# Optimization experiments

Hardware: AMD Instinct MI355X
Metric: run time of the kernel (lower is better)

## Reference

```python
import jax, jax.numpy as jnp
import numpy as np

B, T = 16, 64
A = 6              # num_actions
E = 12288          # embed_size
DET = 4096         # deter_size
HID = 1024         # hidden_size
S, D = 32, 32      # stoch_size, discrete
UM = 0.01          # uniform_mix
CLIP = 1.0         # action_clip
EPS = 1e-3         # LayerNorm eps


def _ln(x, g, b):
    m = jnp.mean(x, -1, keepdims=True)
    v = jnp.var(x, -1, keepdims=True)
    return (x - m) * jax.lax.rsqrt(v + EPS) * g + b


def setup_inputs() -> dict:
    key = jax.random.key(0)
    ks = jax.random.split(key, 24)
    w = lambda k, i, o: (jax.random.normal(k, (i, o), jnp.float32) / np.sqrt(i))
    gum = lambda k, shp: -jnp.log(-jnp.log(jax.random.uniform(k, shp, jnp.float32, 1e-6, 1.0 - 1e-6)))
    is_firsts = (jax.random.uniform(ks[2], (B, T)) < 0.05).astype(jnp.float32)
    is_firsts = is_firsts.at[:, 0].set(1.0)
    return {
        'embed': jax.random.normal(ks[0], (B, T, E), jnp.float32),
        'prev_actions': jax.random.normal(ks[1], (B, T, A), jnp.float32),
        'is_firsts': is_firsts,
        'gumbel_prior': gum(ks[3], (B, T, S, D)),
        'gumbel_post': gum(ks[4], (B, T, S, D)),
        'w_init': jnp.zeros((DET,), jnp.float32),
        'W_img1': w(ks[5], S * D + A, HID), 'g_img1': jnp.ones((HID,)), 'b_img1': jnp.zeros((HID,)),
        'W_gru': w(ks[6], HID + DET, 3 * DET), 'g_gru': jnp.ones((3 * DET,)), 'b_gru': jnp.zeros((3 * DET,)),
        'W_img2a': w(ks[7], DET, HID), 'g_img2': jnp.ones((HID,)), 'b_img2': jnp.zeros((HID,)),
        'W_img2b': w(ks[8], HID, S * D), 'bb_img2': jnp.zeros((S * D,)),
        'W_obs': w(ks[9], E + DET, HID), 'g_obs': jnp.ones((HID,)), 'b_obs': jnp.zeros((HID,)),
        'W_obsb': w(ks[10], HID, S * D), 'bb_obs': jnp.zeros((S * D,)),
    }


def reference(embed, prev_actions, is_firsts, gumbel_prior, gumbel_post,
              w_init, W_img1, g_img1, b_img1, W_gru, g_gru, b_gru,
              W_img2a, g_img2, b_img2, W_img2b, bb_img2,
              W_obs, g_obs, b_obs, W_obsb, bb_obs):
    sg = jax.lax.stop_gradient

    def clip_act(a):
        return a * sg(CLIP / jnp.maximum(jnp.abs(a), CLIP))

    def prior_logits(deter):  # mlp_img2
        h = jax.nn.silu(_ln(deter @ W_img2a, g_img2, b_img2))
        return (h @ W_img2b + bb_img2).reshape(deter.shape[:-1] + (S, D))

    def mix_probs(logits):  # OneHotDist uniform mix
        p = jax.nn.softmax(logits, -1)
        return (1.0 - UM) * p + UM / D

    def st_sample(logits, g):  # straight-through gumbel-max sample
        p = mix_probs(logits)
        oh = jax.nn.one_hot(jnp.argmax(jnp.log(p) + g, -1), D, dtype=logits.dtype)
        return oh + p - sg(p)

    def st_mode(logits):
        p = mix_probs(logits)
        oh = jax.nn.one_hot(jnp.argmax(p, -1), D, dtype=logits.dtype)
        return oh + p - sg(p)

    # learned initial state (initial(): deter=tanh(w), stoch=mode, logits=0)
    init_deter = jnp.broadcast_to(jnp.tanh(w_init)[None], (B, DET))
    init_stoch = st_mode(prior_logits(init_deter))

    # observe() with prev_state=None zeroes the first action and starts from initial state
    prev_actions = prev_actions.at[:, 0].set(0.0)

    def step(carry, xs):
        stoch, deter, logits_post = carry
        a, e, f, gp, gq = xs
        a = clip_act(a)                                  # clip in forward()
        f1 = f[:, None]
        f3 = f[:, None, None]
        a = a * (1.0 - f1)
        stoch = stoch * (1.0 - f3) + init_stoch * f3
        deter = deter * (1.0 - f1) + init_deter * f1
        logits_post = logits_post * (1.0 - f3)           # initial logits are zeros
        a = clip_act(a)                                  # clipped again in forward_img()
        # mlp_img1
        x = jax.nn.silu(_ln(jnp.concatenate([stoch.reshape(B, S * D), a], -1) @ W_img1, g_img1, b_img1))
        # DreamerV2 GRU cell: single LN-linear -> reset/cand/update
        parts = _ln(jnp.concatenate([x, deter], -1) @ W_gru, g_gru, b_gru)
        reset, cand, update = jnp.split(parts, 3, -1)
        reset = jax.nn.sigmoid(reset)
        cand = jnp.tanh(reset * cand)
        update = jax.nn.sigmoid(update - 1.0)
        deter_new = update * cand + (1.0 - update) * deter
        # prior head
        lp = prior_logits(deter_new)
        stoch_prior = st_sample(lp, gp)
        # posterior head (mlp_obs1)
        h2 = jax.nn.silu(_ln(jnp.concatenate([e, deter_new], -1) @ W_obs, g_obs, b_obs))
        lq = (h2 @ W_obsb + bb_obs).reshape(B, S, D)
        stoch_post = st_sample(lq, gq)
        return (stoch_post, deter_new, lq), (stoch_post, deter_new, lq, stoch_prior, lp)

    carry0 = (init_stoch, init_deter, jnp.zeros((B, S, D), embed.dtype))
    xs = (jnp.swapaxes(prev_actions, 0, 1), jnp.swapaxes(embed, 0, 1), jnp.swapaxes(is_firsts, 0, 1),
          jnp.swapaxes(gumbel_prior, 0, 1), jnp.swapaxes(gumbel_post, 0, 1))
    _, outs = jax.lax.scan(step, carry0, xs)
    post_stoch, post_deter, post_logits, prior_stoch, prior_lg = [jnp.swapaxes(o, 0, 1) for o in outs]
    # pack posts and priors (prior deter == post deter) into one array [B,T,8192]
    return jnp.concatenate([post_stoch.reshape(B, T, S * D), post_deter,
                            post_logits.reshape(B, T, S * D),
                            prior_stoch.reshape(B, T, S * D),
                            prior_lg.reshape(B, T, S * D)], -1)
```

## Files before the change

### kernel.cpp

```cpp
#include <hip/hip_runtime.h>
#include <cmath>


#define B 16
#define T_STEPS 64
#define A_DIM 6
#define E_DIM 12288
#define DET 4096
#define HID 1024
#define SD 1024
#define OUT_C 8192
#define OUT_RSTRIDE (T_STEPS * OUT_C)

typedef float f2v __attribute__((ext_vector_type(2)));

__device__ __forceinline__ float block_sum(float v, float* red, int nw) {
#pragma unroll
  for (int m = 32; m >= 1; m >>= 1) v += __shfl_xor(v, m, 64);
  int wid = threadIdx.x >> 6;
  if ((threadIdx.x & 63) == 0) red[wid] = v;
  __syncthreads();
  if (wid == 0) {
    float s = ((int)threadIdx.x < nw) ? red[threadIdx.x] : 0.0f;
#pragma unroll
    for (int m = 8; m >= 1; m >>= 1) s += __shfl_xor(s, m, 16);
    if (threadIdx.x == 0) red[0] = s;
  }
  __syncthreads();
  float out = red[0];
  __syncthreads();
  return out;
}

__global__ __launch_bounds__(1024) void k_tanh(const float* __restrict__ w, float* __restrict__ o) {
  int i = blockIdx.x * 1024 + threadIdx.x;
  if (i < DET) o[i] = tanhf(w[i]);
}

__global__ __launch_bounds__(256) void k_prep(
    const float* __restrict__ isf, const float* __restrict__ pa, int t,
    const float* __restrict__ stoch_prev,
    const float* __restrict__ deter_prev, long deter_prev_stride,
    const float* __restrict__ init_stoch, const float* __restrict__ init_deter_row,
    float* __restrict__ stoch_in, float* __restrict__ deter_in, float* __restrict__ a_eff) {
  int r = blockIdx.x;
  float f = isf[r * T_STEPS + t];
  float omf = 1.0f - f;
  for (int c = threadIdx.x; c < SD; c += 256)
    stoch_in[r * SD + c] = stoch_prev[r * SD + c] * omf + init_stoch[r * SD + c] * f;
  for (int c = threadIdx.x; c < DET; c += 256)
    deter_in[r * DET + c] = deter_prev[(long)r * deter_prev_stride + c] * omf + init_deter_row[c] * f;
  if ((int)threadIdx.x < A_DIM) {
    float a = pa[(r * T_STEPS + t) * A_DIM + threadIdx.x];
    a = a * (1.0f / fmaxf(fabsf(a), 1.0f));
    a_eff[r * 8 + threadIdx.x] = a * omf;
  }
}

struct GemmArgs {
  const float* A0; long sA0; int cA0;
  const float* A1; long sA1;
  const float* W; int N; int Ktot; int KS; int nsplit;
  float* P;
};

template <bool NT>
__global__ __launch_bounds__(256) void k_gemm(GemmArgs ga, GemmArgs gb) {
  const GemmArgs g = blockIdx.z ? gb : ga;
  if ((int)blockIdx.y >= g.nsplit) return;
  const int tid = threadIdx.x;
  const int c0 = blockIdx.x * 512 + tid * 2;
  const int k0 = (int)blockIdx.y * g.KS;
  __shared__ float in_s[16][64];
  float acc[16][2];
#pragma unroll
  for (int r = 0; r < 16; r++) { acc[r][0] = 0.f; acc[r][1] = 0.f; }
  for (int kb = 0; kb < g.KS; kb += 64) {
    const int kbase = k0 + kb;
#pragma unroll
    for (int j = 0; j < 4; j++) {
      int ii = tid + j * 256;
      int r = ii >> 6, kk = ii & 63;
      int k = kbase + kk;
      float v = 0.f;
      if (k < g.cA0) v = g.A0[(long)r * g.sA0 + k];
      else if (k < g.Ktot) v = g.A1[(long)r * g.sA1 + (k - g.cA0)];
      in_s[r][kk] = v;
    }
    __syncthreads();
    if (kbase + 64 <= g.Ktot) {
      const float* wp = g.W + (size_t)kbase * g.N + c0;
#pragma unroll 4
      for (int kk = 0; kk < 64; kk++) {
        f2v w = NT ? __builtin_nontemporal_load((const f2v*)wp) : *(const f2v*)wp;
        wp += g.N;
#pragma unroll
        for (int r = 0; r < 16; r++) {
          float iv = in_s[r][kk];
          acc[r][0] += iv * w[0]; acc[r][1] += iv * w[1];
        }
      }
    } else {
#pragma unroll 4
      for (int kk = 0; kk < 64; kk++) {
        int krow = kbase + kk; if (krow >= g.Ktot) krow = g.Ktot - 1;
        const f2v w = *(const f2v*)(g.W + (size_t)krow * g.N + c0);
#pragma unroll
        for (int r = 0; r < 16; r++) {
          float iv = in_s[r][kk];
          acc[r][0] += iv * w[0]; acc[r][1] += iv * w[1];
        }
      }
    }
    __syncthreads();
  }
#pragma unroll
  for (int r = 0; r < 16; r++)
    *(f2v*)(g.P + ((size_t)blockIdx.y * 16 + r) * g.N + c0) = f2v{acc[r][0], acc[r][1]};
}

__global__ __launch_bounds__(256) void k_pre(const float* __restrict__ A,
                                             const float* __restrict__ Bw,
                                             float* __restrict__ ob) {
  __shared__ float As[32][68];
  __shared__ float Bs[32][68];
  const int tid = threadIdx.x;
  const int tx = tid & 15, ty = tid >> 4;
  const int row0 = blockIdx.y * 64, col0 = blockIdx.x * 64;
  const int ar = tid >> 2, ak = (tid & 3) * 8;
  const int bk = tid >> 4, bc = (tid & 15) * 4;
  float acc[4][4] = {};
  const float* ap = A + (size_t)(row0 + ar) * E_DIM + ak;
  const float* bp = Bw + (size_t)bk * HID + col0 + bc;
  for (int k0 = 0; k0 < E_DIM; k0 += 32) {
    float4 a0 = *(const float4*)(ap + k0);
    float4 a1 = *(const float4*)(ap + k0 + 4);
    float4 b0 = *(const float4*)(bp + (size_t)k0 * HID);
    float4 b1 = *(const float4*)(bp + (size_t)(k0 + 16) * HID);
    __syncthreads();
    As[ak + 0][ar] = a0.x; As[ak + 1][ar] = a0.y; As[ak + 2][ar] = a0.z; As[ak + 3][ar] = a0.w;
    As[ak + 4][ar] = a1.x; As[ak + 5][ar] = a1.y; As[ak + 6][ar] = a1.z; As[ak + 7][ar] = a1.w;
    *(float4*)&Bs[bk][bc] = b0;
    *(float4*)&Bs[bk + 16][bc] = b1;
    __syncthreads();
#pragma unroll
    for (int kk = 0; kk < 32; kk++) {
      float4 av = *(const float4*)&As[kk][ty * 4];
      float4 bv = *(const float4*)&Bs[kk][tx * 4];
      acc[0][0] += av.x * bv.x; acc[0][1] += av.x * bv.y; acc[0][2] += av.x * bv.z; acc[0][3] += av.x * bv.w;
      acc[1][0] += av.y * bv.x; acc[1][1] += av.y * bv.y; acc[1][2] += av.y * bv.z; acc[1][3] += av.y * bv.w;
      acc[2][0] += av.z * bv.x; acc[2][1] += av.z * bv.y; acc[2][2] += av.z * bv.z; acc[2][3] += av.z * bv.w;
      acc[3][0] += av.w * bv.x; acc[3][1] += av.w * bv.y; acc[3][2] += av.w * bv.z; acc[3][3] += av.w * bv.w;
    }
  }
#pragma unroll
  for (int i = 0; i < 4; i++)
#pragma unroll
    for (int j = 0; j < 4; j++)
      ob[(size_t)(row0 + ty * 4 + i) * OUT_C + col0 + tx * 4 + j] = acc[i][j];
}

__global__ __launch_bounds__(256) void k_red(const float* __restrict__ P, int nP,
                                             float* __restrict__ S,
                                             float* __restrict__ red_s, float* __restrict__ red_q) {
  int chunk = blockIdx.x, r = blockIdx.y;
  int c = chunk * 1024 + threadIdx.x * 4;
  float4 s = {0, 0, 0, 0};
  for (int ks = 0; ks < nP; ks++) {
    float4 v = *(const float4*)(P + ((size_t)ks * 16 + r) * (3 * DET) + c);
    s.x += v.x; s.y += v.y; s.z += v.z; s.w += v.w;
  }
  *(float4*)(S + (size_t)r * (3 * DET) + c) = s;
  float sx = (s.x + s.y) + (s.z + s.w);
  float sq = (s.x * s.x + s.y * s.y) + (s.z * s.z + s.w * s.w);
  __shared__ float rbuf[8];
#pragma unroll
  for (int m = 32; m >= 1; m >>= 1) { sx += __shfl_xor(sx, m, 64); sq += __shfl_xor(sq, m, 64); }
  int wid = threadIdx.x >> 6;
  if ((threadIdx.x & 63) == 0) { rbuf[wid] = sx; rbuf[4 + wid] = sq; }
  __syncthreads();
  if (threadIdx.x == 0) {
    red_s[r * 12 + chunk] = (rbuf[0] + rbuf[1]) + (rbuf[2] + rbuf[3]);
    red_q[r * 12 + chunk] = (rbuf[4] + rbuf[5]) + (rbuf[6] + rbuf[7]);
  }
}

__global__ __launch_bounds__(1024) void k_gru_gate(
    const float* __restrict__ S, const float* __restrict__ red_s, const float* __restrict__ red_q,
    const float* __restrict__ g, const float* __restrict__ b,
    float* __restrict__ deter_in, float* __restrict__ deter_new,
    float* __restrict__ out_deter, const float* __restrict__ isf, int t,
    const float* __restrict__ init_deter) {
  int r = blockIdx.x;
  __shared__ float mv[2];
  if (threadIdx.x == 0) {
    float s = 0.f, q = 0.f;
    for (int k2 = 0; k2 < 12; k2++) { s += red_s[r * 12 + k2]; q += red_q[r * 12 + k2]; }
    float m = s * (1.0f / (float)(3 * DET));
    float var = q * (1.0f / (float)(3 * DET)) - m * m;
    mv[0] = m; mv[1] = 1.0f / sqrtf(var + 1e-3f);
  }
  __syncthreads();
  float m = mv[0], rs = mv[1];
  float ft = (t + 1 < T_STEPS) ? isf[r * T_STEPS + t + 1] : 0.0f;
  for (int j = threadIdx.x; j < DET; j += 1024) {
    float lr = (S[(size_t)r * (3 * DET) + j] - m) * rs * g[j] + b[j];
    float lc = (S[(size_t)r * (3 * DET) + j + DET] - m) * rs * g[j + DET] + b[j + DET];
    float lu = (S[(size_t)r * (3 * DET) + j + 2 * DET] - m) * rs * g[j + 2 * DET] + b[j + 2 * DET];
    float rr = 1.0f / (1.0f + expf(-lr));
    float cd = tanhf(rr * lc);
    float uu = 1.0f / (1.0f + expf(-(lu - 1.0f)));
    float dn = uu * cd + (1.0f - uu) * deter_in[r * DET + j];
    deter_new[r * DET + j] = dn;
    out_deter[(size_t)r * OUT_RSTRIDE + j] = dn;
    deter_in[r * DET + j] = dn * (1.0f - ft) + init_deter[j] * ft;
  }
}

__global__ __launch_bounds__(1024) void k_fin2(
    const float* __restrict__ Pa_, int nPa, const float* __restrict__ addA, long adsA,
    const float* __restrict__ gva, const float* __restrict__ bva, float* __restrict__ oa,
    const float* __restrict__ Pb_, int nPb, const float* __restrict__ addB, long adsB,
    const float* __restrict__ gvb, const float* __restrict__ bvb, float* __restrict__ ob) {
  int which = blockIdx.x >> 4, r = blockIdx.x & 15, c = threadIdx.x;
  const float* P = which ? Pb_ : Pa_;
  int nP = which ? nPb : nPa;
  const float* add = which ? addB : addA;
  long ads = which ? adsB : adsA;
  const float* gv = which ? gvb : gva;
  const float* bv = which ? bvb : bva;
  float* o = which ? ob : oa;
  __shared__ float red[18];
  float v = add ? add[(size_t)r * ads + c] : 0.0f;
  for (int ks = 0; ks < nP; ks++) v += P[((size_t)ks * 16 + r) * HID + c];
  float m = block_sum(v, red, 16) * (1.0f / (float)HID);
  float d = v - m;
  float var = block_sum(d * d, red, 16) * (1.0f / (float)HID);
  float rs = 1.0f / sqrtf(var + 1e-3f);
  float y = d * rs * gv[c] + bv[c];
  float s = 1.0f / (1.0f + expf(-y));
  o[r * HID + c] = y * s;
}

__global__ __launch_bounds__(1024) void k_samp(
    const float* __restrict__ P0, const float* __restrict__ bb0,
    const float* __restrict__ gum0, long gs0,
    float* __restrict__ st0, long ss0, float* __restrict__ lg0, long ls0,
    const float* __restrict__ P1, const float* __restrict__ bb1,
    const float* __restrict__ gum1, long gs1,
    float* __restrict__ st1, long ss1, float* __restrict__ lg1, long ls1,
    int nP,
    const float* __restrict__ isf, const float* __restrict__ pa, int t,
    float* __restrict__ stoch_in, float* __restrict__ a_eff,
    const float* __restrict__ init_stoch) {
  int which = blockIdx.x >> 4, r = blockIdx.x & 15, c = threadIdx.x;
  const float* P = which ? P1 : P0;
  const float* bbv = which ? bb1 : bb0;
  const float* gum = which ? gum1 : gum0;
  long gs = which ? gs1 : gs0;
  float* st = which ? st1 : st0;
  long ss = which ? ss1 : ss0;
  float* lg = which ? lg1 : lg0;
  long ls = which ? ls1 : ls0;
  float acc = bbv[c];
  for (int ks = 0; ks < nP; ks++) acc += P[((size_t)ks * 16 + r) * SD + c];
  int d = c & 31;
  float mx = acc;
#pragma unroll
  for (int m = 16; m >= 1; m >>= 1) mx = fmaxf(mx, __shfl_xor(mx, m, 32));
  float e = expf(acc - mx);
  float se = e;
#pragma unroll
  for (int m = 16; m >= 1; m >>= 1) se += __shfl_xor(se, m, 32);
  float p = 0.99f * (e / se) + 3.125e-4f;
  float y = gum ? (logf(p) + gum[(long)r * gs + c]) : p;
  float by = y; int bi = d;
#pragma unroll
  for (int m = 16; m >= 1; m >>= 1) {
    float oy = __shfl_xor(by, m, 32);
    int oi = __shfl_xor(bi, m, 32);
    if (oy > by || (oy == by && oi < bi)) { by = oy; bi = oi; }
  }
  float oh = (d == bi) ? 1.0f : 0.0f;
  float outv = (oh + p) - p;
  st[(long)r * ss + c] = outv;
  if (lg) lg[(long)r * ls + c] = acc;
  if (which && stoch_in) {
    float fn = (t + 1 < T_STEPS) ? isf[r * T_STEPS + t + 1] : 0.0f;
    stoch_in[r * SD + c] = outv * (1.0f - fn) + init_stoch[r * SD + c] * fn;
    if (c < A_DIM) {
      float a = (t + 1 < T_STEPS) ? pa[(r * T_STEPS + t + 1) * A_DIM + c] : 0.0f;
      a = a * (1.0f / fmaxf(fabsf(a), 1.0f));
      a_eff[r * 8 + c] = a * (1.0f - fn);
    }
  }
}

static inline GemmArgs mkargs(const float* A0, long sA0, int cA0,
                              const float* A1, long sA1,
                              const float* W, int N, int Ktot, int KS, int nsplit, float* P) {
  GemmArgs g; g.A0 = A0; g.sA0 = sA0; g.cA0 = cA0; g.A1 = A1; g.sA1 = sA1;
  g.W = W; g.N = N; g.Ktot = Ktot; g.KS = KS; g.nsplit = nsplit; g.P = P;
  return g;
}

extern "C" void kernel_launch(void* const* d_in, const int* in_sizes, int n_in,
                              void* d_out, int out_size, void* d_ws, size_t ws_size,
                              hipStream_t stream) {
  const float* embed  = (const float*)d_in[0];
  const float* pa     = (const float*)d_in[1];
  const float* isf    = (const float*)d_in[2];
  const float* gprior = (const float*)d_in[3];
  const float* gpost  = (const float*)d_in[4];
  const float* w_init = (const float*)d_in[5];
  const float* W1  = (const float*)d_in[6];
  const float* g1  = (const float*)d_in[7];
  const float* b1  = (const float*)d_in[8];
  const float* Wg  = (const float*)d_in[9];
  const float* gg  = (const float*)d_in[10];
  const float* bg  = (const float*)d_in[11];
  const float* W2a = (const float*)d_in[12];
  const float* g2  = (const float*)d_in[13];
  const float* b2  = (const float*)d_in[14];
  const float* W2b = (const float*)d_in[15];
  const float* bb2 = (const float*)d_in[16];
  const float* Wo  = (const float*)d_in[17];
  const float* go  = (const float*)d_in[18];
  const float* bo  = (const float*)d_in[19];
  const float* Wob = (const float*)d_in[20];
  const float* bbo = (const float*)d_in[21];
  float* out = (float*)d_out;
  float* ws  = (float*)d_ws;

  float* Pg    = ws;
  float* Sg    = Pg + 3932160;
  float* red_s = Sg + 196608;
  float* red_q = red_s + 192;
  float* Pa    = red_s + 512;
  float* Pb    = Pa + 524288;
  float* Ps0   = Pb + 524288;
  float* Ps1   = Ps0 + 262144;
  float* Pimg1 = Pa;
  float* st_   = Ps1 + 262144;
  float* init_stoch = st_;
  float* init_deter = st_ + 16384;
  float* stoch_in   = st_ + 20480;
  float* deter_in   = st_ + 36864;
  float* deter_new  = st_ + 102400;
  float* a_eff      = st_ + 167936;
  float* x          = st_ + 168064;
  float* h          = st_ + 184448;
  float* h2         = st_ + 200832;

  GemmArgs Z = mkargs(nullptr, 0, 0, nullptr, 0, nullptr, 1, 0, 64, 0, nullptr);

  k_pre<<<dim3(16, 16), 256, 0, stream>>>(embed, Wo, out + 5120);

  k_tanh<<<4, 1024, 0, stream>>>(w_init, init_deter);
  {
    GemmArgs g = mkargs(init_deter, 0, DET, nullptr, 0, W2a, HID, DET, 128, 32, Pa);
    k_gemm<true><<<dim3(2, 32, 1), 256, 0, stream>>>(g, Z);
  }
  k_fin2<<<16, 1024, 0, stream>>>(Pa, 32, nullptr, 0, g2, b2, h,
                                  Pa, 32, nullptr, 0, g2, b2, h);
  {
    GemmArgs g = mkargs(h, HID, HID, nullptr, 0, W2b, SD, HID, 64, 16, Ps0);
    k_gemm<true><<<dim3(2, 16, 1), 256, 0, stream>>>(g, Z);
  }
  k_samp<<<16, 1024, 0, stream>>>(Ps0, bb2, nullptr, 0, init_stoch, SD, nullptr, 0,
                                  Ps0, bb2, nullptr, 0, init_stoch, SD, nullptr, 0,
                                  16, isf, pa, -1, nullptr, nullptr, init_stoch);

  k_prep<<<16, 256, 0, stream>>>(isf, pa, 0, init_stoch, init_deter, 0,
                                 init_stoch, init_deter, stoch_in, deter_in, a_eff);

  for (int t = 0; t < T_STEPS; t++) {
    {
      GemmArgs g = mkargs(stoch_in, SD, SD, a_eff, 8, W1, HID, SD + A_DIM, 64, 17, Pimg1);
      k_gemm<true><<<dim3(2, 17, 1), 256, 0, stream>>>(g, Z);
    }
    k_fin2<<<16, 1024, 0, stream>>>(Pimg1, 17, nullptr, 0, g1, b1, x,
                                    Pimg1, 17, nullptr, 0, g1, b1, x);
    {
      GemmArgs g = mkargs(x, HID, HID, deter_in, DET, Wg, 3 * DET, HID + DET, 256, 20, Pg);
      k_gemm<false><<<dim3(24, 20, 1), 256, 0, stream>>>(g, Z);
    }
    k_red<<<dim3(12, 16), 256, 0, stream>>>(Pg, 20, Sg, red_s, red_q);
    k_gru_gate<<<16, 1024, 0, stream>>>(Sg, red_s, red_q, gg, bg, deter_in, deter_new,
                                        out + (size_t)t * OUT_C + 1024, isf, t, init_deter);
    {
      GemmArgs gp = mkargs(deter_new, DET, DET, nullptr, 0, W2a, HID, DET, 128, 32, Pa);
      GemmArgs go_ = mkargs(deter_new, DET, DET, nullptr, 0, Wo + (size_t)E_DIM * HID,
                            HID, DET, 128, 32, Pb);
      k_gemm<true><<<dim3(2, 32, 2), 256, 0, stream>>>(gp, go_);
    }
    k_fin2<<<32, 1024, 0, stream>>>(Pa, 32, nullptr, 0, g2, b2, h,
                                    Pb, 32, out + (size_t)t * OUT_C + 5120, OUT_RSTRIDE,
                                    go, bo, h2);
    {
      GemmArgs gs0 = mkargs(h, HID, HID, nullptr, 0, W2b, SD, HID, 64, 16, Ps0);
      GemmArgs gs1 = mkargs(h2, HID, HID, nullptr, 0, Wob, SD, HID, 64, 16, Ps1);
      k_gemm<true><<<dim3(2, 16, 2), 256, 0, stream>>>(gs0, gs1);
    }
    k_samp<<<32, 1024, 0, stream>>>(
        Ps0, bb2, gprior + (size_t)t * SD, (long)T_STEPS * SD,
        out + (size_t)t * OUT_C + 6144, OUT_RSTRIDE,
        out + (size_t)t * OUT_C + 7168, OUT_RSTRIDE,
        Ps1, bbo, gpost + (size_t)t * SD, (long)T_STEPS * SD,
        out + (size_t)t * OUT_C + 0, OUT_RSTRIDE,
        out + (size_t)t * OUT_C + 5120, OUT_RSTRIDE,
        16, isf, pa, t, stoch_in, a_eff, init_stoch);
  }
}
```

Baseline: 10.94 ms.

## Hoist prior head out of recurrent loop into batched post-loop GEMMs

The prior head (W_img2a, LayerNorm, W_img2b and prior sampling) does not feed back into the recurrence, so it is taken out of the per-step loop. After the loop it runs as batched tiled GEMMs over all 1024 (B*T) rows, reading deter from the output buffer. This removes half the per-step weight streaming for the prior path and fuses per-row work into large efficient GEMMs. The GEMM kernel also moves its barrier to the top of the k-loop, raises its unroll factor, and drops the dual-argument dispatch.

```diff
diff --git a/kernel.cpp b/kernel.cpp
--- a/kernel.cpp
+++ b/kernel.cpp
@@ -13,6 +13,7 @@
 #define OUT_RSTRIDE (T_STEPS * OUT_C)
 
 typedef float f2v __attribute__((ext_vector_type(2)));
+typedef float f4v __attribute__((ext_vector_type(4)));
 
 __device__ __forceinline__ float block_sum(float v, float* red, int nw) {
 #pragma unroll
@@ -65,9 +66,7 @@
 };
 
 template <bool NT>
-__global__ __launch_bounds__(256) void k_gemm(GemmArgs ga, GemmArgs gb) {
-  const GemmArgs g = blockIdx.z ? gb : ga;
-  if ((int)blockIdx.y >= g.nsplit) return;
+__global__ __launch_bounds__(256) void k_gemm(GemmArgs g) {
   const int tid = threadIdx.x;
   const int c0 = blockIdx.x * 512 + tid * 2;
   const int k0 = (int)blockIdx.y * g.KS;
@@ -77,6 +76,7 @@
   for (int r = 0; r < 16; r++) { acc[r][0] = 0.f; acc[r][1] = 0.f; }
   for (int kb = 0; kb < g.KS; kb += 64) {
     const int kbase = k0 + kb;
+    __syncthreads();
 #pragma unroll
     for (int j = 0; j < 4; j++) {
       int ii = tid + j * 256;
@@ -90,38 +90,79 @@
     __syncthreads();
     if (kbase + 64 <= g.Ktot) {
       const float* wp = g.W + (size_t)kbase * g.N + c0;
-#pragma unroll 4
+#pragma unroll 8
       for (int kk = 0; kk < 64; kk++) {
         f2v w = NT ? __builtin_nontemporal_load((const f2v*)wp) : *(const f2v*)wp;
         wp += g.N;
 #pragma unroll
         for (int r = 0; r < 16; r++) {
-          float iv = in_s[r][kk];
-          acc[r][0] += iv * w[0]; acc[r][1] += iv * w[1];
+          acc[r][0] += in_s[r][kk] * w[0]; acc[r][1] += in_s[r][kk] * w[1];
         }
       }
     } else {
-#pragma unroll 4
       for (int kk = 0; kk < 64; kk++) {
         int krow = kbase + kk; if (krow >= g.Ktot) krow = g.Ktot - 1;
         const f2v w = *(const f2v*)(g.W + (size_t)krow * g.N + c0);
 #pragma unroll
         for (int r = 0; r < 16; r++) {
-          float iv = in_s[r][kk];
-          acc[r][0] += iv * w[0]; acc[r][1] += iv * w[1];
+          acc[r][0] += in_s[r][kk] * w[0]; acc[r][1] += in_s[r][kk] * w[1];
         }
       }
     }
-    __syncthreads();
   }
 #pragma unroll
   for (int r = 0; r < 16; r++)
     *(f2v*)(g.P + ((size_t)blockIdx.y * 16 + r) * g.N + c0) = f2v{acc[r][0], acc[r][1]};
 }
 
-__global__ __launch_bounds__(256) void k_pre(const float* __restrict__ A,
-                                             const float* __restrict__ Bw,
-                                             float* __restrict__ ob) {
+__global__ __launch_bounds__(1024) void k_fin(
+    const float* __restrict__ P, int nP,
+    const float* __restrict__ add, long ads,
+    const float* __restrict__ gv, const float* __restrict__ bv,
+    float* __restrict__ o) {
+  int r = blockIdx.x, c = threadIdx.x;
+  __shared__ float red[18];
+  float v = add ? add[(size_t)r * ads + c] : 0.0f;
+  for (int ks = 0; ks < nP; ks++) v += P[((size_t)ks * 16 + r) * HID + c];
+  float m = block_sum(v, red, 16) * (1.0f / (float)HID);
+  float d = v - m;
+  float var = block_sum(d * d, red, 16) * (1.0f / (float)HID);
+  float rs = 1.0f / sqrtf(var + 1e-3f);
+  float y = d * rs * gv[c] + bv[c];
+  float s = 1.0f / (1.0f + expf(-y));
+  o[r * HID + c] = y * s;
+}
+
+__global__ __launch_bounds__(1024) void k_samp_init(
+    const float* __restrict__ P, int nP, const float* __restrict__ bb,
+    float* __restrict__ st) {
+  int r = blockIdx.x, c = threadIdx.x;
+  float acc = bb[c];
+  for (int ks = 0; ks < nP; ks++) acc += P[((size_t)ks * 16 + r) * SD + c];
+  int d = c & 31;
+  float mx = acc;
+#pragma unroll
+  for (int m = 16; m >= 1; m >>= 1) mx = fmaxf(mx, __shfl_xor(mx, m, 32));
+  float e = expf(acc - mx);
+  float se = e;
+#pragma unroll
+  for (int m = 16; m >= 1; m >>= 1) se += __shfl_xor(se, m, 32);
+  float p = 0.99f * (e / se) + 3.125e-4f;
+  float by = p; int bi = d;
+#pragma unroll
+  for (int m = 16; m >= 1; m >>= 1) {
+    float oy = __shfl_xor(by, m, 32);
+    int oi = __shfl_xor(bi, m, 32);
+    if (oy > by || (oy == by && oi < bi)) { by = oy; bi = oi; }
+  }
+  float oh = (d == bi) ? 1.0f : 0.0f;
+  st[r * SD + c] = (oh + p) - p;
+}
+
+__global__ __launch_bounds__(256) void k_mm(const float* __restrict__ A, long lda,
+                                            const float* __restrict__ Bw, int K,
+                                            float* __restrict__ out, long ldo,
+                                            const float* __restrict__ bias) {
   __shared__ float As[32][68];
   __shared__ float Bs[32][68];
   const int tid = threadIdx.x;
@@ -130,9 +171,9 @@
   const int ar = tid >> 2, ak = (tid & 3) * 8;
   const int bk = tid >> 4, bc = (tid & 15) * 4;
   float acc[4][4] = {};
-  const float* ap = A + (size_t)(row0 + ar) * E_DIM + ak;
+  const float* ap = A + (size_t)(row0 + ar) * lda + ak;
   const float* bp = Bw + (size_t)bk * HID + col0 + bc;
-  for (int k0 = 0; k0 < E_DIM; k0 += 32) {
+  for (int k0 = 0; k0 < K; k0 += 32) {
     float4 a0 = *(const float4*)(ap + k0);
     float4 a1 = *(const float4*)(ap + k0 + 4);
     float4 b0 = *(const float4*)(bp + (size_t)k0 * HID);
@@ -154,10 +195,60 @@
     }
   }
 #pragma unroll
-  for (int i = 0; i < 4; i++)
-#pragma unroll
-    for (int j = 0; j < 4; j++)
-      ob[(size_t)(row0 + ty * 4 + i) * OUT_C + col0 + tx * 4 + j] = acc[i][j];
+  for (int i = 0; i < 4; i++) {
+    float4 o;
+    int col = col0 + tx * 4;
+    o.x = acc[i][0] + (bias ? bias[col + 0] : 0.f);
+    o.y = acc[i][1] + (bias ? bias[col + 1] : 0.f);
+    o.z = acc[i][2] + (bias ? bias[col + 2] : 0.f);
+    o.w = acc[i][3] + (bias ? bias[col + 3] : 0.f);
+    *(float4*)(out + (size_t)(row0 + ty * 4 + i) * ldo + col) = o;
+  }
+}
+
+__global__ __launch_bounds__(256) void k_ln_rows(float* __restrict__ h,
+                                                 const float* __restrict__ gv,
+                                                 const float* __restrict__ bv) {
+  int row = blockIdx.x, c0 = threadIdx.x * 4;
+  __shared__ float red[18];
+  float4 v = *(const float4*)(h + (size_t)row * HID + c0);
+  float lsum = (v.x + v.y) + (v.z + v.w);
+  float m = block_sum(lsum, red, 4) * (1.0f / (float)HID);
+  float dx = v.x - m, dy = v.y - m, dz = v.z - m, dw = v.w - m;
+  float lv = (dx * dx + dy * dy) + (dz * dz + dw * dw);
+  float var = block_sum(lv, red, 4) * (1.0f / (float)HID);
+  float rs = 1.0f / sqrtf(var + 1e-3f);
+  float4 o;
+  float y0 = dx * rs * gv[c0] + bv[c0];         o.x = y0 / (1.0f + expf(-y0));
+  float y1 = dy * rs * gv[c0 + 1] + bv[c0 + 1]; o.y = y1 / (1.0f + expf(-y1));
+  float y2 = dz * rs * gv[c0 + 2] + bv[c0 + 2]; o.z = y2 / (1.0f + expf(-y2));
+  float y3 = dw * rs * gv[c0 + 3] + bv[c0 + 3]; o.w = y3 / (1.0f + expf(-y3));
+  *(float4*)(h + (size_t)row * HID + c0) = o;
+}
+
+__global__ __launch_bounds__(1024) void k_samp_prior(float* __restrict__ out,
+                                                     const float* __restrict__ gum) {
+  int m = blockIdx.x, c = threadIdx.x;
+  float lp = out[(size_t)m * OUT_C + 7168 + c];
+  int d = c & 31;
+  float mx = lp;
+#pragma unroll
+  for (int mm = 16; mm >= 1; mm >>= 1) mx = fmaxf(mx, __shfl_xor(mx, mm, 32));
+  float e = expf(lp - mx);
+  float se = e;
+#pragma unroll
+  for (int mm = 16; mm >= 1; mm >>= 1) se += __shfl_xor(se, mm, 32);
+  float p = 0.99f * (e / se) + 3.125e-4f;
+  float y = logf(p) + gum[(size_t)m * SD + c];
+  float by = y; int bi = d;
+#pragma unroll
+  for (int mm = 16; mm >= 1; mm >>= 1) {
+    float oy = __shfl_xor(by, mm, 32);
+    int oi = __shfl_xor(bi, mm, 32);
+    if (oy > by || (oy == by && oi < bi)) { by = oy; bi = oi; }
+  }
+  float oh = (d == bi) ? 1.0f : 0.0f;
+  out[(size_t)m * OUT_C + 6144 + c] = (oh + p) - p;
 }
 
 __global__ __launch_bounds__(256) void k_red(const float* __restrict__ P, int nP,
@@ -217,52 +308,15 @@
   }
 }
 
-__global__ __launch_bounds__(1024) void k_fin2(
-    const float* __restrict__ Pa_, int nPa, const float* __restrict__ addA, long adsA,
-    const float* __restrict__ gva, const float* __restrict__ bva, float* __restrict__ oa,
-    const float* __restrict__ Pb_, int nPb, const float* __restrict__ addB, long adsB,
-    const float* __restrict__ gvb, const float* __restrict__ bvb, float* __restrict__ ob) {
-  int which = blockIdx.x >> 4, r = blockIdx.x & 15, c = threadIdx.x;
-  const float* P = which ? Pb_ : Pa_;
-  int nP = which ? nPb : nPa;
-  const float* add = which ? addB : addA;
-  long ads = which ? adsB : adsA;
-  const float* gv = which ? gvb : gva;
-  const float* bv = which ? bvb : bva;
-  float* o = which ? ob : oa;
-  __shared__ float red[18];
-  float v = add ? add[(size_t)r * ads + c] : 0.0f;
-  for (int ks = 0; ks < nP; ks++) v += P[((size_t)ks * 16 + r) * HID + c];
-  float m = block_sum(v, red, 16) * (1.0f / (float)HID);
-  float d = v - m;
-  float var = block_sum(d * d, red, 16) * (1.0f / (float)HID);
-  float rs = 1.0f / sqrtf(var + 1e-3f);
-  float y = d * rs * gv[c] + bv[c];
-  float s = 1.0f / (1.0f + expf(-y));
-  o[r * HID + c] = y * s;
-}
-
 __global__ __launch_bounds__(1024) void k_samp(
-    const float* __restrict__ P0, const float* __restrict__ bb0,
-    const float* __restrict__ gum0, long gs0,
-    float* __restrict__ st0, long ss0, float* __restrict__ lg0, long ls0,
-    const float* __restrict__ P1, const float* __restrict__ bb1,
-    const float* __restrict__ gum1, long gs1,
-    float* __restrict__ st1, long ss1, float* __restrict__ lg1, long ls1,
-    int nP,
+    const float* __restrict__ P, int nP, const float* __restrict__ bb,
+    const float* __restrict__ gum, long gs,
+    float* __restrict__ st, long ss, float* __restrict__ lg, long ls,
     const float* __restrict__ isf, const float* __restrict__ pa, int t,
     float* __restrict__ stoch_in, float* __restrict__ a_eff,
     const float* __restrict__ init_stoch) {
-  int which = blockIdx.x >> 4, r = blockIdx.x & 15, c = threadIdx.x;
-  const float* P = which ? P1 : P0;
-  const float* bbv = which ? bb1 : bb0;
-  const float* gum = which ? gum1 : gum0;
-  long gs = which ? gs1 : gs0;
-  float* st = which ? st1 : st0;
-  long ss = which ? ss1 : ss0;
-  float* lg = which ? lg1 : lg0;
-  long ls = which ? ls1 : ls0;
-  float acc = bbv[c];
+  int r = blockIdx.x, c = threadIdx.x;
+  float acc = bb[c];
   for (int ks = 0; ks < nP; ks++) acc += P[((size_t)ks * 16 + r) * SD + c];
   int d = c & 31;
   float mx = acc;
@@ -273,7 +327,7 @@
 #pragma unroll
   for (int m = 16; m >= 1; m >>= 1) se += __shfl_xor(se, m, 32);
   float p = 0.99f * (e / se) + 3.125e-4f;
-  float y = gum ? (logf(p) + gum[(long)r * gs + c]) : p;
+  float y = logf(p) + gum[(long)r * gs + c];
   float by = y; int bi = d;
 #pragma unroll
   for (int m = 16; m >= 1; m >>= 1) {
@@ -284,15 +338,13 @@
   float oh = (d == bi) ? 1.0f : 0.0f;
   float outv = (oh + p) - p;
   st[(long)r * ss + c] = outv;
-  if (lg) lg[(long)r * ls + c] = acc;
-  if (which && stoch_in) {
-    float fn = (t + 1 < T_STEPS) ? isf[r * T_STEPS + t + 1] : 0.0f;
-    stoch_in[r * SD + c] = outv * (1.0f - fn) + init_stoch[r * SD + c] * fn;
-    if (c < A_DIM) {
-      float a = (t + 1 < T_STEPS) ? pa[(r * T_STEPS + t + 1) * A_DIM + c] : 0.0f;
-      a = a * (1.0f / fmaxf(fabsf(a), 1.0f));
-      a_eff[r * 8 + c] = a * (1.0f - fn);
-    }
+  lg[(long)r * ls + c] = acc;
+  float fn = (t + 1 < T_STEPS) ? isf[r * T_STEPS + t + 1] : 0.0f;
+  stoch_in[r * SD + c] = outv * (1.0f - fn) + init_stoch[r * SD + c] * fn;
+  if (c < A_DIM) {
+    float a = (t + 1 < T_STEPS) ? pa[(r * T_STEPS + t + 1) * A_DIM + c] : 0.0f;
+    a = a * (1.0f / fmaxf(fabsf(a), 1.0f));
+    a_eff[r * 8 + c] = a * (1.0f - fn);
   }
 }
 
@@ -333,14 +385,13 @@
   float* ws  = (float*)d_ws;
 
   float* Pg    = ws;
+  float* h_all = Pg;
   float* Sg    = Pg + 3932160;
   float* red_s = Sg + 196608;
   float* red_q = red_s + 192;
-  float* Pa    = red_s + 512;
-  float* Pb    = Pa + 524288;
-  float* Ps0   = Pb + 524288;
-  float* Ps1   = Ps0 + 262144;
-  float* Pimg1 = Pa;
+  float* Pimg1 = red_s + 512;
+  float* Pb    = Pimg1 + 278528;
+  float* Ps1   = Pb + 524288;
   float* st_   = Ps1 + 262144;
   float* init_stoch = st_;
   float* init_deter = st_ + 16384;
@@ -349,66 +400,45 @@
   float* deter_new  = st_ + 102400;
   float* a_eff      = st_ + 167936;
   float* x          = st_ + 168064;
-  float* h          = st_ + 184448;
-  float* h2         = st_ + 200832;
-
-  GemmArgs Z = mkargs(nullptr, 0, 0, nullptr, 0, nullptr, 1, 0, 64, 0, nullptr);
-
-  k_pre<<<dim3(16, 16), 256, 0, stream>>>(embed, Wo, out + 5120);
+  float* h2         = st_ + 184448;
+
+  k_mm<<<dim3(16, 16), 256, 0, stream>>>(embed, E_DIM, Wo, E_DIM, out + 5120, OUT_C, nullptr);
 
   k_tanh<<<4, 1024, 0, stream>>>(w_init, init_deter);
-  {
-    GemmArgs g = mkargs(init_deter, 0, DET, nullptr, 0, W2a, HID, DET, 128, 32, Pa);
-    k_gemm<true><<<dim3(2, 32, 1), 256, 0, stream>>>(g, Z);
-  }
-  k_fin2<<<16, 1024, 0, stream>>>(Pa, 32, nullptr, 0, g2, b2, h,
-                                  Pa, 32, nullptr, 0, g2, b2, h);
-  {
-    GemmArgs g = mkargs(h, HID, HID, nullptr, 0, W2b, SD, HID, 64, 16, Ps0);
-    k_gemm<true><<<dim3(2, 16, 1), 256, 0, stream>>>(g, Z);
-  }
-  k_samp<<<16, 1024, 0, stream>>>(Ps0, bb2, nullptr, 0, init_stoch, SD, nullptr, 0,
-                                  Ps0, bb2, nullptr, 0, init_stoch, SD, nullptr, 0,
-                                  16, isf, pa, -1, nullptr, nullptr, init_stoch);
+  k_gemm<true><<<dim3(2, 32), 256, 0, stream>>>(
+      mkargs(init_deter, 0, DET, nullptr, 0, W2a, HID, DET, 128, 32, Pb));
+  k_fin<<<16, 1024, 0, stream>>>(Pb, 32, nullptr, 0, g2, b2, x);
+  k_gemm<true><<<dim3(2, 16), 256, 0, stream>>>(
+      mkargs(x, HID, HID, nullptr, 0, W2b, SD, HID, 64, 16, Ps1));
+  k_samp_init<<<16, 1024, 0, stream>>>(Ps1, 16, bb2, init_stoch);
 
   k_prep<<<16, 256, 0, stream>>>(isf, pa, 0, init_stoch, init_deter, 0,
                                  init_stoch, init_deter, stoch_in, deter_in, a_eff);
 
   for (int t = 0; t < T_STEPS; t++) {
-    {
-      GemmArgs g = mkargs(stoch_in, SD, SD, a_eff, 8, W1, HID, SD + A_DIM, 64, 17, Pimg1);
-      k_gemm<true><<<dim3(2, 17, 1), 256, 0, stream>>>(g, Z);
-    }
-    k_fin2<<<16, 1024, 0, stream>>>(Pimg1, 17, nullptr, 0, g1, b1, x,
-                                    Pimg1, 17, nullptr, 0, g1, b1, x);
-    {
-      GemmArgs g = mkargs(x, HID, HID, deter_in, DET, Wg, 3 * DET, HID + DET, 256, 20, Pg);
-      k_gemm<false><<<dim3(24, 20, 1), 256, 0, stream>>>(g, Z);
-    }
+    k_gemm<true><<<dim3(2, 17), 256, 0, stream>>>(
+        mkargs(stoch_in, SD, SD, a_eff, 8, W1, HID, SD + A_DIM, 64, 17, Pimg1));
+    k_fin<<<16, 1024, 0, stream>>>(Pimg1, 17, nullptr, 0, g1, b1, x);
+    k_gemm<false><<<dim3(24, 20), 256, 0, stream>>>(
+        mkargs(x, HID, HID, deter_in, DET, Wg, 3 * DET, HID + DET, 256, 20, Pg));
     k_red<<<dim3(12, 16), 256, 0, stream>>>(Pg, 20, Sg, red_s, red_q);
     k_gru_gate<<<16, 1024, 0, stream>>>(Sg, red_s, red_q, gg, bg, deter_in, deter_new,
                                         out + (size_t)t * OUT_C + 1024, isf, t, init_deter);
-    {
-      GemmArgs gp = mkargs(deter_new, DET, DET, nullptr, 0, W2a, HID, DET, 128, 32, Pa);
-      GemmArgs go_ = mkargs(deter_new, DET, DET, nullptr, 0, Wo + (size_t)E_DIM * HID,
-                            HID, DET, 128, 32, Pb);
-      k_gemm<true><<<dim3(2, 32, 2), 256, 0, stream>>>(gp, go_);
-    }
-    k_fin2<<<32, 1024, 0, stream>>>(Pa, 32, nullptr, 0, g2, b2, h,
-                                    Pb, 32, out + (size_t)t * OUT_C + 5120, OUT_RSTRIDE,
-                                    go, bo, h2);
-    {
-      GemmArgs gs0 = mkargs(h, HID, HID, nullptr, 0, W2b, SD, HID, 64, 16, Ps0);
-      GemmArgs gs1 = mkargs(h2, HID, HID, nullptr, 0, Wob, SD, HID, 64, 16, Ps1);
-      k_gemm<true><<<dim3(2, 16, 2), 256, 0, stream>>>(gs0, gs1);
-    }
-    k_samp<<<32, 1024, 0, stream>>>(
-        Ps0, bb2, gprior + (size_t)t * SD, (long)T_STEPS * SD,
-        out + (size_t)t * OUT_C + 6144, OUT_RSTRIDE,
-        out + (size_t)t * OUT_C + 7168, OUT_RSTRIDE,
-        Ps1, bbo, gpost + (size_t)t * SD, (long)T_STEPS * SD,
+    k_gemm<true><<<dim3(2, 32), 256, 0, stream>>>(
+        mkargs(deter_new, DET, DET, nullptr, 0, Wo + (size_t)E_DIM * HID, HID, DET, 128, 32, Pb));
+    k_fin<<<16, 1024, 0, stream>>>(Pb, 32, out + (size_t)t * OUT_C + 5120, OUT_RSTRIDE,
+                                   go, bo, h2);
+    k_gemm<true><<<dim3(2, 16), 256, 0, stream>>>(
+        mkargs(h2, HID, HID, nullptr, 0, Wob, SD, HID, 64, 16, Ps1));
+    k_samp<<<16, 1024, 0, stream>>>(
+        Ps1, 16, bbo, gpost + (size_t)t * SD, (long)T_STEPS * SD,
         out + (size_t)t * OUT_C + 0, OUT_RSTRIDE,
         out + (size_t)t * OUT_C + 5120, OUT_RSTRIDE,
-        16, isf, pa, t, stoch_in, a_eff, init_stoch);
-  }
-}
+        isf, pa, t, stoch_in, a_eff, init_stoch);
+  }
+
+  k_mm<<<dim3(16, 16), 256, 0, stream>>>(out + 1024, OUT_C, W2a, DET, h_all, HID, nullptr);
+  k_ln_rows<<<1024, 256, 0, stream>>>(h_all, g2, b2);
+  k_mm<<<dim3(16, 16), 256, 0, stream>>>(h_all, HID, W2b, HID, out + 7168, OUT_C, bb2);
+  k_samp_prior<<<1024, 1024, 0, stream>>>(out, gprior);
+}
```

New measurement: 18.83 ms. 72.2% more time.
